# Kernel optimization log

Hardware: AMD Instinct MI355X
Metric: run time of the kernel (lower is better)

Reference implementation:

```python
import jax, jax.numpy as jnp
import numpy as np

N = 50000        # nodes
E = 250000       # edges (avg degree 5)
D = 32           # embed_dim
N_LAYERS = 3


def _uniform(key, shape, fan_in):
    s = 1.0 / np.sqrt(fan_in)
    return jax.random.uniform(key, shape, jnp.float32, -s, s)


def setup_inputs() -> dict:
    key = jax.random.key(0)
    ks = jax.random.split(key, 10)
    x = jax.random.normal(ks[0], (N, 1), jnp.float32)
    edge_index = jax.random.randint(ks[1], (2, E), 0, N, dtype=jnp.int64)
    edge_attribute = jax.random.normal(ks[2], (E, 1), jnp.float32)
    # Linear weights stored as [in, out] (i.e. torch weight transposed)
    node_W = _uniform(ks[3], (1, D), 1)
    node_b = _uniform(ks[4], (D,), 1)
    l1_W = _uniform(ks[5], (1, D * D), 1)
    l1_b = _uniform(ks[6], (D * D,), 1)
    root = _uniform(ks[7], (D, D), D)      # NNConv root weight
    conv_b = _uniform(ks[8], (D,), D)      # NNConv bias
    return {
        "x": x, "edge_index": edge_index, "edge_attribute": edge_attribute,
        "i": 2, "dummy": 0,
        "node_W": node_W, "node_b": node_b,
        "l1_W": l1_W, "l1_b": l1_b,
        "root": root, "conv_b": conv_b,
    }


def reference(x, edge_index, edge_attribute, i, dummy, node_W, node_b,
              l1_W, l1_b, root, conv_b):
    n_encode_layers = min(i + 1, N_LAYERS)
    src, dst = edge_index[0], edge_index[1]

    # node embedding: [N,1] -> [N,D]
    h = x @ node_W + node_b

    # edge-conditioned weight matrices, shared by every layer: [E, D, D]
    We = (edge_attribute @ l1_W + l1_b).reshape(E, D, D)

    # mean-aggregation denominator (in-degree, clamped; isolated nodes -> 0 msg)
    cnt = jax.ops.segment_sum(jnp.ones((E,), h.dtype), dst, num_segments=N)
    cnt = jnp.maximum(cnt, 1.0)[:, None]

    for _ in range(n_encode_layers):
        h = jax.nn.relu(h)
        # gather source features, per-edge matmul: msg_e = x_src[e] @ We[e]
        msg = jnp.einsum('ei,eio->eo', h[src], We)
        aggr = jax.ops.segment_sum(msg, dst, num_segments=N) / cnt
        h = aggr + h @ root + conv_b
    return h
```

## Files before the change

### kernel.cpp

```cpp
#include <hip/hip_runtime.h>
#include <hip/hip_bf16.h>

#define N_NODES 50000
#define N_EDGES 250000
#define DIM 32
#define BLK 256
#define CAP 32
#define SPILL_MAX 4096
#define EDGE_NB 977
#define WCONV_NB 13
#define LAYER_NB 1563
#define POISON 0xAAAAAAAAu

typedef __attribute__((ext_vector_type(8))) short short8;
typedef __attribute__((ext_vector_type(4))) float f32x4;

__device__ __forceinline__ float ldf(const void* p, int i, int isf32) {
    return isf32 ? ((const float*)p)[i]
                 : __bfloat162float(((const __hip_bfloat16*)p)[i]);
}
__device__ __forceinline__ float b2f(unsigned short u) {
    return __uint_as_float(((unsigned int)u) << 16);
}
__device__ __forceinline__ int ldi(const int* ei, int i, int i64) {
    return i64 ? ei[2 * i] : ei[i];
}
__device__ __forceinline__ int clamp_idx(int v) {
    v = v < 0 ? 0 : v;
    return v >= N_NODES ? N_NODES - 1 : v;
}
__device__ __forceinline__ bool half_is_big(const void* p, int k) {
    unsigned short h = ((const unsigned short*)p)[k];
    float v = __uint_as_float(((unsigned int)h) << 16);
    return !(fabsf(v) <= 50.0f);
}
__device__ __forceinline__ unsigned short bf16bits(float v) {
    __hip_bfloat16 b = __float2bfloat16(v);
    return __builtin_bit_cast(unsigned short, b);
}

__global__ __launch_bounds__(BLK) void prep_kernel(
    const int* __restrict__ ei, const void* __restrict__ ea,
    const void* __restrict__ lW, const void* __restrict__ lb,
    const void* __restrict__ rt, const void* __restrict__ cb,
    int* __restrict__ cntI, int2* __restrict__ packed,
    int* __restrict__ spill_cnt, int4* __restrict__ spill,
    float* __restrict__ wCB, unsigned short* __restrict__ wfrag)
{
    __shared__ int sdet;
    int tid = threadIdx.x;
    int b = blockIdx.x;
    if (tid == 0) sdet = 0;
    __syncthreads();

    if (b < EDGE_NB) {
        if (tid < 64) {
            if (ei[2 * tid + 1] != 0) atomicOr(&sdet, 2);
        } else if (tid < 192) {
            if (half_is_big(ea, tid - 64)) atomicOr(&sdet, 1);
        }
        __syncthreads();
        int f_ea = sdet & 1, i64 = ((sdet & 2) == 0);
        int e = b * BLK + tid;
        if (e < N_EDGES) {
            int s = clamp_idx(ldi(ei, e, i64));
            int d = clamp_idx(ldi(ei, N_EDGES + e, i64));
            float a = ldf(ea, e, f_ea);
            unsigned k = (unsigned)atomicAdd(&cntI[d], 1) - POISON;
            if (k < CAP) {
                packed[d * CAP + (int)k] = make_int2(s, __float_as_int(a));
            } else {
                unsigned sp = (unsigned)atomicAdd(spill_cnt, 1) - POISON;
                if (sp < SPILL_MAX)
                    spill[sp] = make_int4(d, s, __float_as_int(a), 0);
            }
        }
        return;
    }

    if (tid < 64)       { if (half_is_big(lW, tid) || half_is_big(lW, tid + 64)) atomicOr(&sdet, 1); }
    else if (tid < 128) { int k = tid - 64;  if (half_is_big(lb, k) || half_is_big(lb, k + 64)) atomicOr(&sdet, 2); }
    else if (tid < 192) { int k = tid - 128; if (half_is_big(rt, k) || half_is_big(rt, k + 64)) atomicOr(&sdet, 4); }
    else if (tid < 224) { if (half_is_big(cb, tid - 192)) atomicOr(&sdet, 8); }
    __syncthreads();
    int fW = sdet & 1, fB = sdet & 2, fR = sdet & 4, fC = sdet & 8;
    int g = (int)(b - EDGE_NB) * BLK + tid;
    if (g < 3072) {
        int f = g >> 9, rem = g & 511;
        int ln = rem >> 3, j = rem & 7;
        int t = f >> 1, nh = f & 1;
        int k = t * 32 + (ln >> 4) * 8 + j;
        int n = nh * 16 + (ln & 15);
        float v;
        if (k < 32)      v = ldf(lW, k * 32 + n, fW);
        else if (k < 64) v = ldf(lb, (k - 32) * 32 + n, fB);
        else             v = ldf(rt, (k - 64) * 32 + n, fR);
        wfrag[g] = bf16bits(v);
    } else if (g < 3104) {
        wCB[g - 3072] = ldf(cb, g - 3072, fC);
    }
}

__global__ __launch_bounds__(512) void layer_kernel(
    const int2* __restrict__ packed, const int* __restrict__ cntI,
    const int* __restrict__ spill_cnt, const int4* __restrict__ spill,
    const void* __restrict__ x, const void* __restrict__ nW,
    const void* __restrict__ nb,
    const unsigned short* __restrict__ hin, const float* __restrict__ wCB,
    const unsigned short* __restrict__ wfrag,
    void* __restrict__ outb, int mode0, int last)
{
    __shared__ __align__(16) unsigned short sAu[32 * 96];
    __shared__ int sdet;
    int tid = threadIdx.x;
    int wv = tid >> 6;
    int lane = tid & 63;
    int half = lane >> 5;
    int l32 = lane & 31;
    int nbase = blockIdx.x * 32;
    int n0 = nbase + wv * 4;

    float nWl = 0.0f, nbl = 0.0f;
    int f_x = 0;
    if (mode0) {
        if (tid == 0) sdet = 0;
        __syncthreads();
        if (tid < 128) {
            if (half_is_big(x, tid)) atomicOr(&sdet, 4);
        } else if (tid < 160) {
            if (half_is_big(nW, tid - 128)) atomicOr(&sdet, 8);
        } else if (tid < 192) {
            if (half_is_big(nb, tid - 160)) atomicOr(&sdet, 16);
        }
        __syncthreads();
        f_x = sdet & 4;
        nWl = ldf(nW, l32, sdet & 8);
        nbl = ldf(nb, l32, sdet & 16);
    }

    int deg[4];
    if (n0 + 3 < N_NODES) {
        int4 d4 = *(const int4*)(cntI + n0);
        deg[0] = (int)((unsigned)d4.x - POISON);
        deg[1] = (int)((unsigned)d4.y - POISON);
        deg[2] = (int)((unsigned)d4.z - POISON);
        deg[3] = (int)((unsigned)d4.w - POISON);
    } else {
        #pragma unroll
        for (int j = 0; j < 4; ++j) {
            int n = n0 + j;
            deg[j] = (n < N_NODES) ? (int)((unsigned)cntI[n] - POISON) : 0;
        }
    }

    float hl01, hl23;
    if (mode0) {
        int na = clamp_idx(n0 + half), nc = clamp_idx(n0 + 2 + half);
        float xa = ldf(x, na, f_x), xc = ldf(x, nc, f_x);
        hl01 = fmaf(xa, nWl, nbl); hl01 = hl01 > 0.0f ? hl01 : 0.0f;
        hl23 = fmaf(xc, nWl, nbl); hl23 = hl23 > 0.0f ? hl23 : 0.0f;
    } else {
        hl01 = b2f(hin[n0 * DIM + lane]);
        hl23 = b2f(hin[(n0 + 2) * DIM + lane]);
    }

    int2 c[4][4];
    #pragma unroll
    for (int j = 0; j < 4; ++j) {
        int base = (n0 + j) * CAP;
        #pragma unroll
        for (int i = 0; i < 4; ++i)
            c[j][i] = packed[base + 2 * i + half];
    }
    float h[4][4];
    #pragma unroll
    for (int j = 0; j < 4; ++j) {
        #pragma unroll
        for (int i = 0; i < 4; ++i) {
            int src = ((2 * i + half) < deg[j]) ? c[j][i].x : 0;
            if (mode0) {
                float xs = ldf(x, src, f_x);
                float hv = fmaf(xs, nWl, nbl);
                h[j][i] = hv > 0.0f ? hv : 0.0f;
            } else {
                h[j][i] = b2f(hin[src * DIM + l32]);
            }
        }
    }
    float p[4] = {0, 0, 0, 0}, q[4] = {0, 0, 0, 0};
    #pragma unroll
    for (int j = 0; j < 4; ++j) {
        #pragma unroll
        for (int i = 0; i < 4; ++i) {
            bool valid = (2 * i + half) < deg[j];
            float hv = valid ? h[j][i] : 0.0f;
            float a  = valid ? __int_as_float(c[j][i].y) : 0.0f;
            p[j] = fmaf(a, hv, p[j]);
            q[j] += hv;
        }
    }
    #pragma unroll
    for (int j = 0; j < 4; ++j) {
        int dgc = deg[j] < CAP ? deg[j] : CAP;
        for (int k = 8 + half; k < dgc; k += 2) {
            int2 cc = packed[(n0 + j) * CAP + k];
            float hv;
            if (mode0) {
                float xs = ldf(x, cc.x, f_x);
                hv = fmaf(xs, nWl, nbl);
                hv = hv > 0.0f ? hv : 0.0f;
            } else {
                hv = b2f(hin[cc.x * DIM + l32]);
            }
            p[j] = fmaf(__int_as_float(cc.y), hv, p[j]);
            q[j] += hv;
        }
    }
    unsigned spt = (unsigned)(*spill_cnt) - POISON;
    if (spt != 0) {
        if (spt > SPILL_MAX) spt = SPILL_MAX;
        #pragma unroll
        for (int j = 0; j < 4; ++j) {
            if (deg[j] > CAP) {
                for (unsigned t = (unsigned)half; t < spt; t += 2) {
                    int4 sp = spill[t];
                    if (sp.x == n0 + j) {
                        float hv;
                        if (mode0) {
                            float xs = ldf(x, sp.y, f_x);
                            hv = fmaf(xs, nWl, nbl);
                            hv = hv > 0.0f ? hv : 0.0f;
                        } else {
                            hv = b2f(hin[sp.y * DIM + l32]);
                        }
                        p[j] = fmaf(__int_as_float(sp.z), hv, p[j]);
                        q[j] += hv;
                    }
                }
            }
        }
    }
    #pragma unroll
    for (int j = 0; j < 4; ++j) {
        p[j] += __shfl_xor(p[j], 32);
        q[j] += __shfl_xor(q[j], 32);
        float ic = 1.0f / (deg[j] < 1 ? 1.0f : (float)deg[j]);
        p[j] *= ic;
        q[j] *= ic;
    }
    #pragma unroll
    for (int j = 0; j < 4; ++j)
        sAu[(wv * 4 + j) * 96 + half * 32 + l32] = bf16bits(half ? q[j] : p[j]);
    sAu[(wv * 4 + half) * 96 + 64 + l32] = bf16bits(hl01);
    sAu[(wv * 4 + 2 + half) * 96 + 64 + l32] = bf16bits(hl23);
    __syncthreads();

    if (wv < 4) {
        int rg = wv & 1, nh = wv >> 1;
        short8 bfr[3];
        #pragma unroll
        for (int t = 0; t < 3; ++t)
            bfr[t] = *(const short8*)(wfrag + ((t * 2 + nh) * 64 + lane) * 8);
        f32x4 acc = {0.0f, 0.0f, 0.0f, 0.0f};
        #pragma unroll
        for (int t = 0; t < 3; ++t) {
            short8 afr = *(const short8*)(sAu + (rg * 16 + (lane & 15)) * 96
                                          + t * 32 + (lane >> 4) * 8);
            acc = __builtin_amdgcn_mfma_f32_16x16x32_bf16(afr, bfr[t], acc, 0, 0, 0);
        }
        float cbl = wCB[nh * 16 + (lane & 15)];
        #pragma unroll
        for (int r = 0; r < 4; ++r) {
            int row = rg * 16 + (lane >> 4) * 4 + r;
            int n = nbase + row;
            if (n < N_NODES) {
                float v = acc[r] + cbl;
                if (!last) {
                    v = v > 0.0f ? v : 0.0f;
                    ((unsigned short*)outb)[n * DIM + nh * 16 + (lane & 15)] =
                        bf16bits(v);
                } else {
                    ((float*)outb)[n * DIM + nh * 16 + (lane & 15)] = v;
                }
            }
        }
    }
}

extern "C" void kernel_launch(void* const* d_in, const int* in_sizes, int n_in,
                              void* d_out, int out_size, void* d_ws, size_t ws_size,
                              hipStream_t stream) {
    const void* p[16];
    int np_ = 0;
    for (int i = 0; i < n_in && np_ < 16; ++i)
        if (in_sizes[i] != 1) p[np_++] = d_in[i];

    const void* x      = p[0];
    const int*  ei     = (const int*)p[1];
    const void* ea     = p[2];
    const void* node_W = p[3];
    const void* node_b = p[4];
    const void* l1_W   = p[5];
    const void* l1_b   = p[6];
    const void* root   = p[7];
    const void* conv_b = p[8];
    float* out = (float*)d_out;

    const int ND = N_NODES * DIM;
    char* ws = (char*)d_ws;
    int2*  packed    = (int2*)ws;
    unsigned short* hr1 = (unsigned short*)(packed + N_NODES * CAP);
    unsigned short* hr2 = hr1 + ND;
    float* wCB       = (float*)(hr2 + ND);
    unsigned short* wfrag = (unsigned short*)(wCB + 32);
    int*   cntI      = (int*)(wfrag + 3072);
    int*   spill_cnt = cntI + N_NODES;
    int4*  spill     = (int4*)(spill_cnt + 4);

    prep_kernel<<<EDGE_NB + WCONV_NB, BLK, 0, stream>>>(
        ei, ea, l1_W, l1_b, root, conv_b,
        cntI, packed, spill_cnt, spill, wCB, wfrag);

    layer_kernel<<<LAYER_NB, 512, 0, stream>>>(packed, cntI, spill_cnt, spill,
        x, node_W, node_b, hr2 , wCB, wfrag, hr1, 1, 0);
    layer_kernel<<<LAYER_NB, 512, 0, stream>>>(packed, cntI, spill_cnt, spill,
        x, node_W, node_b, hr1, wCB, wfrag, hr2, 0, 0);
    layer_kernel<<<LAYER_NB, 512, 0, stream>>>(packed, cntI, spill_cnt, spill,
        x, node_W, node_b, hr2, wCB, wfrag, out, 0, 1);
}
```

Baseline: 159.1 us.

## Gather node features as packed bf16 pairs with 16-lane quarters and halve edge CAP

Reorganizes the per-node gather so each wave quarter handles two edges and each lane reads a 32-bit word holding two bf16 features, using int4 loads of packed edge records. It also shrinks the per-node edge slot capacity from 32 to 16, so the packed buffer is smaller and more high-degree nodes go through the spill path. The intent is fewer, wider memory transactions and less edge-list traffic, at the cost of extra cross-lane reductions and a slower spill scan for nodes with more than 16 in-edges.

```diff
diff --git a/kernel.cpp b/kernel.cpp
--- a/kernel.cpp
+++ b/kernel.cpp
@@ -5,7 +5,7 @@
 #define N_EDGES 250000
 #define DIM 32
 #define BLK 256
-#define CAP 32
+#define CAP 16
 #define SPILL_MAX 4096
 #define EDGE_NB 977
 #define WCONV_NB 13
@@ -19,8 +19,8 @@
     return isf32 ? ((const float*)p)[i]
                  : __bfloat162float(((const __hip_bfloat16*)p)[i]);
 }
-__device__ __forceinline__ float b2f(unsigned short u) {
-    return __uint_as_float(((unsigned int)u) << 16);
+__device__ __forceinline__ float b2f(unsigned int u16) {
+    return __uint_as_float(u16 << 16);
 }
 __device__ __forceinline__ int ldi(const int* ei, int i, int i64) {
     return i64 ? ei[2 * i] : ei[i];
@@ -37,6 +37,9 @@
 __device__ __forceinline__ unsigned short bf16bits(float v) {
     __hip_bfloat16 b = __float2bfloat16(v);
     return __builtin_bit_cast(unsigned short, b);
+}
+__device__ __forceinline__ unsigned int pack2(float lo, float hi) {
+    return ((unsigned int)bf16bits(hi) << 16) | (unsigned int)bf16bits(lo);
 }
 
 __global__ __launch_bounds__(BLK) void prep_kernel(
@@ -106,21 +109,22 @@
     const int* __restrict__ spill_cnt, const int4* __restrict__ spill,
     const void* __restrict__ x, const void* __restrict__ nW,
     const void* __restrict__ nb,
-    const unsigned short* __restrict__ hin, const float* __restrict__ wCB,
+    const unsigned int* __restrict__ hin,
+    const float* __restrict__ wCB,
     const unsigned short* __restrict__ wfrag,
     void* __restrict__ outb, int mode0, int last)
 {
-    __shared__ __align__(16) unsigned short sAu[32 * 96];
+    __shared__ __align__(16) unsigned int sAu32[32 * 48];
     __shared__ int sdet;
     int tid = threadIdx.x;
     int wv = tid >> 6;
     int lane = tid & 63;
-    int half = lane >> 5;
-    int l32 = lane & 31;
+    int q = lane >> 4;
+    int l16 = lane & 15;
     int nbase = blockIdx.x * 32;
     int n0 = nbase + wv * 4;
 
-    float nWl = 0.0f, nbl = 0.0f;
+    float nW2lo = 0.0f, nW2hi = 0.0f, nb2lo = 0.0f, nb2hi = 0.0f;
     int f_x = 0;
     if (mode0) {
         if (tid == 0) sdet = 0;
@@ -134,9 +138,16 @@
         }
         __syncthreads();
         f_x = sdet & 4;
-        nWl = ldf(nW, l32, sdet & 8);
-        nbl = ldf(nb, l32, sdet & 16);
-    }
+        nW2lo = ldf(nW, 2 * l16,     sdet & 8);
+        nW2hi = ldf(nW, 2 * l16 + 1, sdet & 8);
+        nb2lo = ldf(nb, 2 * l16,     sdet & 16);
+        nb2hi = ldf(nb, 2 * l16 + 1, sdet & 16);
+    }
+
+    int4 c[4];
+    #pragma unroll
+    for (int j = 0; j < 4; ++j)
+        c[j] = *(const int4*)(packed + (n0 + j) * CAP + 2 * q);
 
     int deg[4];
     if (n0 + 3 < N_NODES) {
@@ -153,67 +164,78 @@
         }
     }
 
-    float hl01, hl23;
-    if (mode0) {
-        int na = clamp_idx(n0 + half), nc = clamp_idx(n0 + 2 + half);
-        float xa = ldf(x, na, f_x), xc = ldf(x, nc, f_x);
-        hl01 = fmaf(xa, nWl, nbl); hl01 = hl01 > 0.0f ? hl01 : 0.0f;
-        hl23 = fmaf(xc, nWl, nbl); hl23 = hl23 > 0.0f ? hl23 : 0.0f;
-    } else {
-        hl01 = b2f(hin[n0 * DIM + lane]);
-        hl23 = b2f(hin[(n0 + 2) * DIM + lane]);
-    }
-
-    int2 c[4][4];
+    float hslo, hshi;
+    {
+        int ns = clamp_idx(n0 + q);
+        if (mode0) {
+            float xs = ldf(x, ns, f_x);
+            hslo = fmaf(xs, nW2lo, nb2lo); hslo = hslo > 0.0f ? hslo : 0.0f;
+            hshi = fmaf(xs, nW2hi, nb2hi); hshi = hshi > 0.0f ? hshi : 0.0f;
+        } else {
+            unsigned int u = hin[ns * 16 + l16];
+            hslo = b2f(u & 0xffffu);
+            hshi = b2f(u >> 16);
+        }
+    }
+
+    float plo[4] = {0,0,0,0}, phi[4] = {0,0,0,0};
+    float qlo[4] = {0,0,0,0}, qhi[4] = {0,0,0,0};
     #pragma unroll
     for (int j = 0; j < 4; ++j) {
-        int base = (n0 + j) * CAP;
-        #pragma unroll
-        for (int i = 0; i < 4; ++i)
-            c[j][i] = packed[base + 2 * i + half];
-    }
-    float h[4][4];
+        int s0 = clamp_idx(c[j].x), s1 = clamp_idx(c[j].z);
+        float a0 = __int_as_float(c[j].y), a1 = __int_as_float(c[j].w);
+        float h0lo, h0hi, h1lo, h1hi;
+        if (mode0) {
+            float xs0 = ldf(x, s0, f_x), xs1 = ldf(x, s1, f_x);
+            h0lo = fmaf(xs0, nW2lo, nb2lo); h0lo = h0lo > 0.0f ? h0lo : 0.0f;
+            h0hi = fmaf(xs0, nW2hi, nb2hi); h0hi = h0hi > 0.0f ? h0hi : 0.0f;
+            h1lo = fmaf(xs1, nW2lo, nb2lo); h1lo = h1lo > 0.0f ? h1lo : 0.0f;
+            h1hi = fmaf(xs1, nW2hi, nb2hi); h1hi = h1hi > 0.0f ? h1hi : 0.0f;
+        } else {
+            unsigned int u0 = hin[s0 * 16 + l16];
+            unsigned int u1 = hin[s1 * 16 + l16];
+            h0lo = b2f(u0 & 0xffffu); h0hi = b2f(u0 >> 16);
+            h1lo = b2f(u1 & 0xffffu); h1hi = b2f(u1 >> 16);
+        }
+        bool v0 = (2 * q)     < deg[j];
+        bool v1 = (2 * q + 1) < deg[j];
+        float a0m = v0 ? a0 : 0.0f, a1m = v1 ? a1 : 0.0f;
+        float h0lom = v0 ? h0lo : 0.0f, h0him = v0 ? h0hi : 0.0f;
+        float h1lom = v1 ? h1lo : 0.0f, h1him = v1 ? h1hi : 0.0f;
+        plo[j] = fmaf(a0m, h0lom, plo[j]); plo[j] = fmaf(a1m, h1lom, plo[j]);
+        phi[j] = fmaf(a0m, h0him, phi[j]); phi[j] = fmaf(a1m, h1him, phi[j]);
+        qlo[j] += h0lom + h1lom;
+        qhi[j] += h0him + h1him;
+    }
     #pragma unroll
     for (int j = 0; j < 4; ++j) {
-        #pragma unroll
-        for (int i = 0; i < 4; ++i) {
-            int src = ((2 * i + half) < deg[j]) ? c[j][i].x : 0;
+        if (deg[j] > 8) {
+            int4 c2 = *(const int4*)(packed + (n0 + j) * CAP + 8 + 2 * q);
+            int dgc = deg[j] < CAP ? deg[j] : CAP;
+            int s0 = clamp_idx(c2.x), s1 = clamp_idx(c2.z);
+            float a0 = __int_as_float(c2.y), a1 = __int_as_float(c2.w);
+            float h0lo, h0hi, h1lo, h1hi;
             if (mode0) {
-                float xs = ldf(x, src, f_x);
-                float hv = fmaf(xs, nWl, nbl);
-                h[j][i] = hv > 0.0f ? hv : 0.0f;
+                float xs0 = ldf(x, s0, f_x), xs1 = ldf(x, s1, f_x);
+                h0lo = fmaf(xs0, nW2lo, nb2lo); h0lo = h0lo > 0.0f ? h0lo : 0.0f;
+                h0hi = fmaf(xs0, nW2hi, nb2hi); h0hi = h0hi > 0.0f ? h0hi : 0.0f;
+                h1lo = fmaf(xs1, nW2lo, nb2lo); h1lo = h1lo > 0.0f ? h1lo : 0.0f;
+                h1hi = fmaf(xs1, nW2hi, nb2hi); h1hi = h1hi > 0.0f ? h1hi : 0.0f;
             } else {
-                h[j][i] = b2f(hin[src * DIM + l32]);
+                unsigned int u0 = hin[s0 * 16 + l16];
+                unsigned int u1 = hin[s1 * 16 + l16];
+                h0lo = b2f(u0 & 0xffffu); h0hi = b2f(u0 >> 16);
+                h1lo = b2f(u1 & 0xffffu); h1hi = b2f(u1 >> 16);
             }
-        }
-    }
-    float p[4] = {0, 0, 0, 0}, q[4] = {0, 0, 0, 0};
-    #pragma unroll
-    for (int j = 0; j < 4; ++j) {
-        #pragma unroll
-        for (int i = 0; i < 4; ++i) {
-            bool valid = (2 * i + half) < deg[j];
-            float hv = valid ? h[j][i] : 0.0f;
-            float a  = valid ? __int_as_float(c[j][i].y) : 0.0f;
-            p[j] = fmaf(a, hv, p[j]);
-            q[j] += hv;
-        }
-    }
-    #pragma unroll
-    for (int j = 0; j < 4; ++j) {
-        int dgc = deg[j] < CAP ? deg[j] : CAP;
-        for (int k = 8 + half; k < dgc; k += 2) {
-            int2 cc = packed[(n0 + j) * CAP + k];
-            float hv;
-            if (mode0) {
-                float xs = ldf(x, cc.x, f_x);
-                hv = fmaf(xs, nWl, nbl);
-                hv = hv > 0.0f ? hv : 0.0f;
-            } else {
-                hv = b2f(hin[cc.x * DIM + l32]);
-            }
-            p[j] = fmaf(__int_as_float(cc.y), hv, p[j]);
-            q[j] += hv;
+            bool v0 = (8 + 2 * q)     < dgc;
+            bool v1 = (8 + 2 * q + 1) < dgc;
+            float a0m = v0 ? a0 : 0.0f, a1m = v1 ? a1 : 0.0f;
+            float h0lom = v0 ? h0lo : 0.0f, h0him = v0 ? h0hi : 0.0f;
+            float h1lom = v1 ? h1lo : 0.0f, h1him = v1 ? h1hi : 0.0f;
+            plo[j] = fmaf(a0m, h0lom, plo[j]); plo[j] = fmaf(a1m, h1lom, plo[j]);
+            phi[j] = fmaf(a0m, h0him, phi[j]); phi[j] = fmaf(a1m, h1him, phi[j]);
+            qlo[j] += h0lom + h1lom;
+            qhi[j] += h0him + h1him;
         }
     }
     unsigned spt = (unsigned)(*spill_cnt) - POISON;
@@ -222,19 +244,22 @@
         #pragma unroll
         for (int j = 0; j < 4; ++j) {
             if (deg[j] > CAP) {
-                for (unsigned t = (unsigned)half; t < spt; t += 2) {
+                for (unsigned t = (unsigned)q; t < spt; t += 4) {
                     int4 sp = spill[t];
                     if (sp.x == n0 + j) {
-                        float hv;
+                        float hvlo, hvhi;
                         if (mode0) {
-                            float xs = ldf(x, sp.y, f_x);
-                            hv = fmaf(xs, nWl, nbl);
-                            hv = hv > 0.0f ? hv : 0.0f;
+                            float xs = ldf(x, clamp_idx(sp.y), f_x);
+                            hvlo = fmaf(xs, nW2lo, nb2lo); hvlo = hvlo > 0.0f ? hvlo : 0.0f;
+                            hvhi = fmaf(xs, nW2hi, nb2hi); hvhi = hvhi > 0.0f ? hvhi : 0.0f;
                         } else {
-                            hv = b2f(hin[sp.y * DIM + l32]);
+                            unsigned int u = hin[clamp_idx(sp.y) * 16 + l16];
+                            hvlo = b2f(u & 0xffffu); hvhi = b2f(u >> 16);
                         }
-                        p[j] = fmaf(__int_as_float(sp.z), hv, p[j]);
-                        q[j] += hv;
+                        float a = __int_as_float(sp.z);
+                        plo[j] = fmaf(a, hvlo, plo[j]);
+                        phi[j] = fmaf(a, hvhi, phi[j]);
+                        qlo[j] += hvlo; qhi[j] += hvhi;
                     }
                 }
             }
@@ -242,20 +267,24 @@
     }
     #pragma unroll
     for (int j = 0; j < 4; ++j) {
-        p[j] += __shfl_xor(p[j], 32);
-        q[j] += __shfl_xor(q[j], 32);
+        plo[j] += __shfl_xor(plo[j], 16); plo[j] += __shfl_xor(plo[j], 32);
+        phi[j] += __shfl_xor(phi[j], 16); phi[j] += __shfl_xor(phi[j], 32);
+        qlo[j] += __shfl_xor(qlo[j], 16); qlo[j] += __shfl_xor(qlo[j], 32);
+        qhi[j] += __shfl_xor(qhi[j], 16); qhi[j] += __shfl_xor(qhi[j], 32);
+    }
+    #pragma unroll
+    for (int j = 0; j < 4; ++j) {
         float ic = 1.0f / (deg[j] < 1 ? 1.0f : (float)deg[j]);
-        p[j] *= ic;
-        q[j] *= ic;
-    }
-    #pragma unroll
-    for (int j = 0; j < 4; ++j)
-        sAu[(wv * 4 + j) * 96 + half * 32 + l32] = bf16bits(half ? q[j] : p[j]);
-    sAu[(wv * 4 + half) * 96 + 64 + l32] = bf16bits(hl01);
-    sAu[(wv * 4 + 2 + half) * 96 + 64 + l32] = bf16bits(hl23);
+        if (q == 0)
+            sAu32[(wv * 4 + j) * 48 + l16]      = pack2(plo[j] * ic, phi[j] * ic);
+        else if (q == 1)
+            sAu32[(wv * 4 + j) * 48 + 16 + l16] = pack2(qlo[j] * ic, qhi[j] * ic);
+    }
+    sAu32[(wv * 4 + q) * 48 + 32 + l16] = pack2(hslo, hshi);
     __syncthreads();
 
     if (wv < 4) {
+        const unsigned short* sAu = (const unsigned short*)sAu32;
         int rg = wv & 1, nh = wv >> 1;
         short8 bfr[3];
         #pragma unroll
@@ -275,12 +304,12 @@
             int n = nbase + row;
             if (n < N_NODES) {
                 float v = acc[r] + cbl;
+                int col = nh * 16 + (lane & 15);
                 if (!last) {
                     v = v > 0.0f ? v : 0.0f;
-                    ((unsigned short*)outb)[n * DIM + nh * 16 + (lane & 15)] =
-                        bf16bits(v);
+                    ((unsigned short*)outb)[n * DIM + col] = bf16bits(v);
                 } else {
-                    ((float*)outb)[n * DIM + nh * 16 + (lane & 15)] = v;
+                    ((float*)outb)[n * DIM + col] = v;
                 }
             }
         }
@@ -309,9 +338,9 @@
     const int ND = N_NODES * DIM;
     char* ws = (char*)d_ws;
     int2*  packed    = (int2*)ws;
-    unsigned short* hr1 = (unsigned short*)(packed + N_NODES * CAP);
-    unsigned short* hr2 = hr1 + ND;
-    float* wCB       = (float*)(hr2 + ND);
+    unsigned int* hr1 = (unsigned int*)(packed + N_NODES * CAP);
+    unsigned int* hr2 = hr1 + N_NODES * 16;
+    float* wCB       = (float*)(hr2 + N_NODES * 16);
     unsigned short* wfrag = (unsigned short*)(wCB + 32);
     int*   cntI      = (int*)(wfrag + 3072);
     int*   spill_cnt = cntI + N_NODES;
```

Result: faster. 136.5 us (-14.2%).
